# Kernel optimization log

Hardware: AMD Instinct MI355X
Metric: run time of the kernel (lower is better)

Reference implementation:

```python
import jax, jax.numpy as jnp
from jax import lax
import numpy as np

N = 4
ALPHA_AP = 0.85
ALPHA_DS = 0.1
ALPHA_LR = 1.0
C1 = 0.01 ** 2
C2 = 0.03 ** 2


def resize_ac(img, nh, nw):
    # bilinear resize, align_corners=True (matches F.interpolate(..., align_corners=True))
    B, C, H, W = img.shape
    ys = jnp.linspace(0.0, H - 1.0, nh)
    xs = jnp.linspace(0.0, W - 1.0, nw)
    y0 = jnp.floor(ys).astype(jnp.int32)
    y1 = jnp.minimum(y0 + 1, H - 1)
    x0 = jnp.floor(xs).astype(jnp.int32)
    x1 = jnp.minimum(x0 + 1, W - 1)
    wy = (ys - y0).astype(img.dtype)[None, None, :, None]
    wx = (xs - x0).astype(img.dtype)[None, None, None, :]
    top = img[:, :, y0, :] * (1.0 - wy) + img[:, :, y1, :] * wy
    return top[:, :, :, x0] * (1.0 - wx) + top[:, :, :, x1] * wx


def build_pyramid(img):
    B, C, H, W = img.shape
    pyr = [img]
    for i in range(N - 1):
        r = 2 ** (i + 1)
        pyr.append(resize_ac(pyr[i], H // r, W // r))  # resize previous level, as in torch code
    return pyr


def x_grad(img):
    # replicate-pad right then diff -> last column is exactly zero
    g = img[:, :, :, :-1] - img[:, :, :, 1:]
    return jnp.concatenate([g, jnp.zeros_like(img[:, :, :, :1])], axis=3)


def y_grad(img):
    g = img[:, :, :-1, :] - img[:, :, 1:, :]
    return jnp.concatenate([g, jnp.zeros_like(img[:, :, :1, :])], axis=2)


def avgpool3(x):
    # AvgPool2d(3, 1), VALID padding
    return lax.reduce_window(x, 0.0, lax.add, (1, 1, 3, 3), (1, 1, 1, 1), 'VALID') / 9.0


def grid_sample_zeros(img, gx, gy):
    # bilinear grid_sample, padding_mode='zeros', align_corners=True
    B, C, H, W = img.shape
    x = (gx + 1.0) * 0.5 * (W - 1)
    y = (gy + 1.0) * 0.5 * (H - 1)
    x0 = jnp.floor(x)
    y0 = jnp.floor(y)

    def corner(xi, yi, w):
        valid = (xi >= 0) & (xi <= W - 1) & (yi >= 0) & (yi <= H - 1)
        xc = jnp.clip(xi, 0, W - 1).astype(jnp.int32)
        yc = jnp.clip(yi, 0, H - 1).astype(jnp.int32)
        vals = jax.vmap(lambda im, yy, xx: im[:, yy, xx])(img, yc, xc)  # [B,C,H,W]
        return vals * (w * valid.astype(img.dtype))[:, None]

    return (corner(x0, y0, (x0 + 1 - x) * (y0 + 1 - y))
            + corner(x0 + 1, y0, (x - x0) * (y0 + 1 - y))
            + corner(x0, y0 + 1, (x0 + 1 - x) * (y - y0))
            + corner(x0 + 1, y0 + 1, (x - x0) * (y - y0)))


def apply_disparity(img, disp):
    # standard Monodepth bilinear sampler: shift x_base in [0,1] by disp, grid_sample
    B, C, H, W = img.shape
    x_base = jnp.linspace(0.0, 1.0, W)[None, None, :]
    y_base = jnp.linspace(0.0, 1.0, H)[None, :, None]
    gx = 2.0 * (x_base + disp[:, 0]) - 1.0  # [B,H,W]
    gy = jnp.broadcast_to(2.0 * y_base - 1.0, gx.shape)
    return grid_sample_zeros(img, gx, gy)


def dssim(x, y):
    mu_x = avgpool3(x)
    mu_y = avgpool3(y)
    sig_x = avgpool3(x * x) - mu_x ** 2
    sig_y = avgpool3(y * y) - mu_y ** 2
    cov = avgpool3(x * y) - mu_x * mu_y
    ssim = ((2.0 * mu_x * mu_y + C1) * (2.0 * cov + C2)) / ((mu_x ** 2 + mu_y ** 2 + C1) * (sig_x + sig_y + C2))
    return jnp.mean(jnp.clip((1.0 - ssim) / 2.0, 0.0, 1.0))


def smoothness(disp, img, level):
    wx = jnp.exp(-jnp.mean(jnp.abs(x_grad(img)), axis=1, keepdims=True))
    wy = jnp.exp(-jnp.mean(jnp.abs(y_grad(img)), axis=1, keepdims=True))
    sx = x_grad(disp) * wx
    sy = y_grad(disp) * wy
    return jnp.mean(jnp.abs(sx) + jnp.abs(sy)) / (2 ** level)


def loss_forward(disps, left, right):
    lp = build_pyramid(left)
    rp = build_pyramid(right)
    dl = [d[:, 0:1] for d in disps]
    dr = [d[:, 1:2] for d in disps]
    left_est = [apply_disparity(rp[i], -dl[i]) for i in range(N)]
    right_est = [apply_disparity(lp[i], dr[i]) for i in range(N)]
    r2l_disp = [apply_disparity(dr[i], -dl[i]) for i in range(N)]
    l2r_disp = [apply_disparity(dl[i], dr[i]) for i in range(N)]
    # appearance matching (note: outer *ALPHA_AP matches the original's AP_loss*self.alpha_AP)
    AP = sum(ALPHA_AP * dssim(lp[i], left_est[i]) + (1.0 - ALPHA_AP) * jnp.mean(jnp.abs(lp[i] - left_est[i])) for i in range(N))
    AP = AP + sum(ALPHA_AP * dssim(rp[i], right_est[i]) + (1.0 - ALPHA_AP) * jnp.mean(jnp.abs(rp[i] - right_est[i])) for i in range(N))
    AP = AP * ALPHA_AP
    LR = sum(jnp.mean(jnp.abs(dl[i] - r2l_disp[i])) for i in range(N))
    LR = (LR + sum(jnp.mean(jnp.abs(dr[i] - l2r_disp[i])) for i in range(N))) * ALPHA_LR
    DS = sum(smoothness(dl[i], lp[i], i) for i in range(N))
    DS = (DS + sum(smoothness(dr[i], rp[i], i) for i in range(N))) * ALPHA_DS
    total = AP + LR + DS
    return total, AP, LR, DS


def setup_inputs() -> dict:
    key = jax.random.key(0)
    ks = jax.random.split(key, 6)
    B, H, W = 32, 256, 512
    inp = {}
    for i in range(N):
        h, w = H >> i, W >> i
        # normalized disparities in [0, 0.05) as in trained Monodepth
        inp[f'disp{i}'] = jax.random.uniform(ks[i], (B, 2, h, w), jnp.float32) * 0.05
    inp['left'] = jax.random.uniform(ks[4], (B, 3, H, W), jnp.float32)
    inp['right'] = jax.random.uniform(ks[5], (B, 3, H, W), jnp.float32)
    return inp


def reference(disp0, disp1, disp2, disp3, left, right):
    return loss_forward([disp0, disp1, disp2, disp3], left, right)
```

## Files before the change

### kernel.cpp

```cpp
#include <hip/hip_runtime.h>

#define BDIM 256
#define SH 16

struct LevelDesc {
    const float* lp; const float* rp; const float* dp;
    int H, W, nCW, nRS, nPerSide, waveBase;
};
struct AllParams { LevelDesc lv[4]; int totalWaves; };

__global__ void zero_acc_kernel(double* acc) {
    if (threadIdx.x < 32) acc[threadIdx.x] = 0.0;
}

__global__ void resize2_kernel(const float* __restrict__ sL, const float* __restrict__ sR,
                               float* __restrict__ dL, float* __restrict__ dR,
                               int BC, int Hs, int Ws, int Hd, int Wd) {
    long long half = (long long)BC * Hd * Wd;
    long long idx = (long long)blockIdx.x * blockDim.x + threadIdx.x;
    if (idx >= 2 * half) return;
    const float* src = (idx < half) ? sL : sR;
    float* dst = (idx < half) ? dL : dR;
    long long id = (idx < half) ? idx : idx - half;
    int i = (int)(id % Wd);
    long long t = id / Wd;
    int j = (int)(t % Hd);
    int bc = (int)(t / Hd);
    float stepy = (float)(Hs - 1) / (float)(Hd - 1);
    float stepx = (float)(Ws - 1) / (float)(Wd - 1);
    float y = j * stepy;
    float x = i * stepx;
    int y0 = (int)floorf(y);
    int y1 = min(y0 + 1, Hs - 1);
    int x0 = (int)floorf(x);
    int x1 = min(x0 + 1, Ws - 1);
    float wy = y - (float)y0;
    float wx = x - (float)x0;
    const float* s = src + (long long)bc * Hs * Ws;
    float t0 = s[(long long)y0 * Ws + x0] * (1.0f - wy) + s[(long long)y1 * Ws + x0] * wy;
    float t1 = s[(long long)y0 * Ws + x1] * (1.0f - wy) + s[(long long)y1 * Ws + x1] * wy;
    dst[id] = t0 * (1.0f - wx) + t1 * wx;
}

__device__ __forceinline__ float ssim_term(float Sx, float Sy, float Sxx, float Syy, float Sxy) {
    const float C1v = 0.0001f;
    const float C2v = 0.0009f;
    float mux = Sx * (1.0f / 9.0f), muy = Sy * (1.0f / 9.0f);
    float sigx = Sxx * (1.0f / 9.0f) - mux * mux;
    float sigy = Syy * (1.0f / 9.0f) - muy * muy;
    float cov  = Sxy * (1.0f / 9.0f) - mux * muy;
    float num = (2.0f * mux * muy + C1v) * (2.0f * cov + C2v);
    float den = (mux * mux + muy * muy + C1v) * (sigx + sigy + C2v);
    float v = (1.0f - num * __builtin_amdgcn_rcpf(den)) * 0.5f;
    return fminf(fmaxf(v, 0.0f), 1.0f);
}

__global__ void __launch_bounds__(BDIM)
mega_kernel(AllParams P, double* __restrict__ acc) {
    const int lane = threadIdx.x & 63;
    const int wid  = threadIdx.x >> 6;
    const int wId  = blockIdx.x * (BDIM / 64) + wid;
    const int w = min(wId, P.totalWaves - 1);

    int level = 0;
    if (w >= P.lv[1].waveBase) level = 1;
    if (w >= P.lv[2].waveBase) level = 2;
    if (w >= P.lv[3].waveBase) level = 3;
    LevelDesc L;
    if (level == 0) L = P.lv[0];
    else if (level == 1) L = P.lv[1];
    else if (level == 2) L = P.lv[2];
    else L = P.lv[3];

    int rel = w - L.waveBase;
    const int side = (rel >= L.nPerSide) ? 1 : 0;
    rel -= side * L.nPerSide;
    const int cw = rel % L.nCW; rel /= L.nCW;
    const int rs = rel % L.nRS;
    const int b  = rel / L.nRS;

    const int H = L.H, W = L.W;
    const long long HW = (long long)H * W;
    const float Wm1f = (float)(W - 1);
    const float sgn = side ? 1.0f : -1.0f;

    const float* xim = (side ? L.rp : L.lp) + (long long)b * 3 * HW;
    const float* sim = (side ? L.lp : L.rp) + (long long)b * 3 * HW;
    const float* dme = L.dp + (long long)b * 2 * HW + (side ? HW : 0);
    const float* dot = L.dp + (long long)b * 2 * HW + (side ? 0 : HW);

    const int base = cw * 126;
    const int c0 = base + 2 * lane;
    const int c1 = c0 + 1;
    const bool in0 = c0 < W, in1 = c1 < W;
    const int cc = min(c0, W - 2) >> 1;
    const float fc0 = (float)c0, fc1 = (float)c1;

    const bool lastW = (cw == L.nCW - 1);
    const bool own0 = in0 && (c0 < base + 126 || lastW);
    const bool own1 = in1 && (c1 < base + 126 || lastW);
    const bool ownS0 = own0 && (c0 <= W - 3);
    const bool ownS1 = own1 && (c1 <= W - 3);

    const int r0 = rs * SH;
    const int r1 = min(r0 + SH, H);
    const int jend = min(r1 + 1, H - 1);

    float Pst[3][5][2], Lst[3][5][2];
#pragma unroll
    for (int c = 0; c < 3; ++c)
#pragma unroll
        for (int s = 0; s < 5; ++s) { Pst[c][s][0] = 0.f; Pst[c][s][1] = 0.f;
                                      Lst[c][s][0] = 0.f; Lst[c][s][1] = 0.f; }
    float pd0 = 0.f, pd1 = 0.f;
    float pxv[3][2] = {{0.f,0.f},{0.f,0.f},{0.f,0.f}};

    float f_ss = 0.f, f_l1 = 0.f, f_lr = 0.f, f_ds = 0.f;

    for (int j = r0; j <= jend; ++j) {
        const long long ro = (long long)j * W;
        float2 dpair = ((const float2*)(dme + ro))[cc];
        float d0 = dpair.x, d1 = dpair.y;

        float xq0 = fmaf(sgn * d0, Wm1f, fc0);
        float xq1 = fmaf(sgn * d1, Wm1f, fc1);
        float xf0 = floorf(xq0), xf1 = floorf(xq1);
        int g0 = (int)xf0, g1 = (int)xf1;
        float t0 = xq0 - xf0, t1 = xq1 - xf1;
        float w00 = (g0 >= 0 && g0 < W)         ? 1.0f - t0 : 0.0f;
        float w01 = (g0 >= -1 && g0 < W - 1)    ? t0        : 0.0f;
        float w10 = (g1 >= 0 && g1 < W)         ? 1.0f - t1 : 0.0f;
        float w11 = (g1 >= -1 && g1 < W - 1)    ? t1        : 0.0f;
        int a0 = min(max(g0, 0), W - 1);
        int a1 = min(max(g0 + 1, 0), W - 1);
        int b0 = min(max(g1, 0), W - 1);
        int b1 = min(max(g1 + 1, 0), W - 1);

        const float* dor = dot + ro;
        float wv0 = dor[a0] * w00 + dor[a1] * w01;
        float wv1 = dor[b0] * w10 + dor[b1] * w11;

        float xv[3][2], yv[3][2];
#pragma unroll
        for (int c = 0; c < 3; ++c) {
            const float* xr = xim + (long long)c * HW + ro;
            const float* sr = sim + (long long)c * HW + ro;
            float2 xp2 = ((const float2*)xr)[cc];
            xv[c][0] = in0 ? xp2.x : 0.f;
            xv[c][1] = in1 ? xp2.y : 0.f;
            yv[c][0] = sr[a0] * w00 + sr[a1] * w01;
            yv[c][1] = sr[b0] * w10 + sr[b1] * w11;
            if (!in0) yv[c][0] = 0.f;
            if (!in1) yv[c][1] = 0.f;
        }

        const bool rowOwn = j < r1;
        if (rowOwn) {
            if (own0) {
                f_l1 += fabsf(xv[0][0] - yv[0][0]) + fabsf(xv[1][0] - yv[1][0]) + fabsf(xv[2][0] - yv[2][0]);
                f_lr += fabsf(d0 - wv0);
            }
            if (own1) {
                f_l1 += fabsf(xv[0][1] - yv[0][1]) + fabsf(xv[1][1] - yv[1][1]) + fabsf(xv[2][1] - yv[2][1]);
                f_lr += fabsf(d1 - wv1);
            }
        }

        {
            float dn  = __shfl_down(d0, 1);
            float xn0 = __shfl_down(xv[0][0], 1);
            float xn1 = __shfl_down(xv[1][0], 1);
            float xn2 = __shfl_down(xv[2][0], 1);
            if (rowOwn) {
                if (own0 && c0 < W - 1) {
                    float g = fabsf(xv[0][0] - xv[0][1]) + fabsf(xv[1][0] - xv[1][1]) + fabsf(xv[2][0] - xv[2][1]);
                    f_ds += fabsf((d0 - d1) * __expf(-g * (1.0f / 3.0f)));
                }
                if (own1 && c1 < W - 1) {
                    float g = fabsf(xv[0][1] - xn0) + fabsf(xv[1][1] - xn1) + fabsf(xv[2][1] - xn2);
                    f_ds += fabsf((d1 - dn) * __expf(-g * (1.0f / 3.0f)));
                }
            }
        }
        if (j > r0 && (j - 1) < r1) {
            if (own0) {
                float g = fabsf(pxv[0][0] - xv[0][0]) + fabsf(pxv[1][0] - xv[1][0]) + fabsf(pxv[2][0] - xv[2][0]);
                f_ds += fabsf((pd0 - d0) * __expf(-g * (1.0f / 3.0f)));
            }
            if (own1) {
                float g = fabsf(pxv[0][1] - xv[0][1]) + fabsf(pxv[1][1] - xv[1][1]) + fabsf(pxv[2][1] - xv[2][1]);
                f_ds += fabsf((pd1 - d1) * __expf(-g * (1.0f / 3.0f)));
            }
        }
        pd0 = d0; pd1 = d1;
#pragma unroll
        for (int c = 0; c < 3; ++c) { pxv[c][0] = xv[c][0]; pxv[c][1] = xv[c][1]; }

        const bool emit = (j >= r0 + 2);
#pragma unroll
        for (int c = 0; c < 3; ++c) {
            float cs[5][2];
#pragma unroll
            for (int p = 0; p < 2; ++p) {
                float cx = xv[c][p], cy = yv[c][p];
                float v5[5] = {cx, cy, cx * cx, cy * cy, cx * cy};
#pragma unroll
                for (int s = 0; s < 5; ++s) {
                    cs[s][p] = Pst[c][s][p] + v5[s];
                    Pst[c][s][p] = Lst[c][s][p] + v5[s];
                    Lst[c][s][p] = v5[s];
                }
            }
            if (emit) {
                float w0s[5], w1s[5];
#pragma unroll
                for (int s = 0; s < 5; ++s) {
                    float n0 = __shfl_down(cs[s][0], 1);
                    float n1 = __shfl_down(cs[s][1], 1);
                    w0s[s] = cs[s][0] + cs[s][1] + n0;
                    w1s[s] = cs[s][1] + n0 + n1;
                }
                float ts0 = ssim_term(w0s[0], w0s[1], w0s[2], w0s[3], w0s[4]);
                float ts1 = ssim_term(w1s[0], w1s[1], w1s[2], w1s[3], w1s[4]);
                f_ss += (ownS0 ? ts0 : 0.f) + (ownS1 ? ts1 : 0.f);
            }
        }
    }

#pragma unroll
    for (int o = 32; o > 0; o >>= 1) {
        f_ss += __shfl_down(f_ss, o);
        f_l1 += __shfl_down(f_l1, o);
        f_lr += __shfl_down(f_lr, o);
        f_ds += __shfl_down(f_ds, o);
    }
    __shared__ float red[BDIM / 64][4];
    __shared__ int meta[2];
    if (threadIdx.x == 0) { meta[0] = level; meta[1] = side; }
    if (lane == 0) {
        red[wid][0] = f_ss; red[wid][1] = f_l1;
        red[wid][2] = f_lr; red[wid][3] = f_ds;
    }
    __syncthreads();
    if (threadIdx.x < 4) {
        int t = threadIdx.x;
        double s = (double)red[0][t] + (double)red[1][t]
                 + (double)red[2][t] + (double)red[3][t];
        atomicAdd(acc + t * 8 + meta[1] * 4 + meta[0], s);
    }
}

__global__ void finalize_kernel(const double* __restrict__ acc, float* __restrict__ out) {
    const int B = 32, H0 = 256, W0 = 512;
    double AP = 0.0, LR = 0.0, DS = 0.0;
    for (int i = 0; i < 4; ++i) {
        int h = H0 >> i, w = W0 >> i;
        double nss = (double)B * 3.0 * (double)(h - 2) * (double)(w - 2);
        double nl1 = (double)B * 3.0 * (double)h * (double)w;
        double nd  = (double)B * (double)h * (double)w;
        AP += 0.85 * (acc[0 + i] / nss) + 0.15 * (acc[8 + i] / nl1);
        AP += 0.85 * (acc[4 + i] / nss) + 0.15 * (acc[12 + i] / nl1);
        LR += acc[16 + i] / nd + acc[20 + i] / nd;
        double sc = 1.0 / (double)(1 << i);
        DS += (acc[24 + i] / nd) * sc + (acc[28 + i] / nd) * sc;
    }
    AP *= 0.85;
    DS *= 0.1;
    double total = AP + LR + DS;
    out[0] = (float)total;
    out[1] = (float)AP;
    out[2] = (float)LR;
    out[3] = (float)DS;
}

extern "C" void kernel_launch(void* const* d_in, const int* in_sizes, int n_in,
                              void* d_out, int out_size, void* d_ws, size_t ws_size,
                              hipStream_t stream) {
    const int B = 32, H0 = 256, W0 = 512;
    const float* dsp[4];
    for (int i = 0; i < 4; ++i) dsp[i] = (const float*)d_in[i];
    const float* left  = (const float*)d_in[4];
    const float* right = (const float*)d_in[5];
    float* out = (float*)d_out;

    double* acc = (double*)d_ws;
    float* buf = (float*)((char*)d_ws + 256);

    const float* lp[4];
    const float* rp[4];
    float* lpm[4];
    float* rpm[4];
    lp[0] = left; rp[0] = right;
    float* cur = buf;
    for (int i = 1; i < 4; ++i) { lpm[i] = cur; cur += (long long)B * 3 * (H0 >> i) * (W0 >> i); }
    for (int i = 1; i < 4; ++i) { rpm[i] = cur; cur += (long long)B * 3 * (H0 >> i) * (W0 >> i); }
    for (int i = 1; i < 4; ++i) { lp[i] = lpm[i]; rp[i] = rpm[i]; }

    zero_acc_kernel<<<1, 64, 0, stream>>>(acc);

    for (int i = 1; i < 4; ++i) {
        int Hs = H0 >> (i - 1), Ws = W0 >> (i - 1);
        int Hd = H0 >> i, Wd = W0 >> i;
        long long half = (long long)B * 3 * Hd * Wd;
        int g = (int)((2 * half + BDIM - 1) / BDIM);
        resize2_kernel<<<g, BDIM, 0, stream>>>(
            lp[i - 1], rp[i - 1], lpm[i], rpm[i], B * 3, Hs, Ws, Hd, Wd);
    }

    AllParams P;
    int wb = 0;
    for (int i = 0; i < 4; ++i) {
        int h = H0 >> i, w = W0 >> i;
        LevelDesc& L = P.lv[i];
        L.lp = lp[i]; L.rp = rp[i]; L.dp = dsp[i];
        L.H = h; L.W = w;
        L.nCW = (w - 2 + 125) / 126;
        L.nRS = h / SH;
        L.nPerSide = B * L.nRS * L.nCW;
        L.waveBase = wb;
        wb += 2 * L.nPerSide;
    }
    P.totalWaves = wb;
    int blocks = (wb + (BDIM / 64) - 1) / (BDIM / 64);
    mega_kernel<<<blocks, BDIM, 0, stream>>>(P, acc);

    finalize_kernel<<<1, 1, 0, stream>>>(acc, out);
}
```

Measured before the change: 302.0 us.

## Software-pipeline row gathers with double-buffered registers and 32-bit indexing

Restructures the per-row loop so the disparity load and all gathers for row j+1 (and the disparity for row j+2) are issued before row j is consumed. Two register sets alternate between rows so memory latency can overlap with the SSIM and smoothness math. Address arithmetic also switches from 64-bit to 32-bit unsigned offsets. The cost is much higher register pressure, which may lower occupancy, and 32-bit offsets assume each tensor slice fits in 4G elements.

Result: slower. 308.6 us (+2.2%).

```diff
diff --git a/kernel.cpp b/kernel.cpp
--- a/kernel.cpp
+++ b/kernel.cpp
@@ -55,6 +55,14 @@
     return fminf(fmaxf(v, 0.0f), 1.0f);
 }
 
+struct RowVals {
+    float d0, d1;
+    float xv[3][2];
+    float w00, w01, w10, w11;
+    float dA, dB, dC, dD;
+    float sA[3], sB[3], sC[3], sD[3];
+};
+
 __global__ void __launch_bounds__(BDIM)
 mega_kernel(AllParams P, double* __restrict__ acc) {
     const int lane = threadIdx.x & 63;
@@ -81,6 +89,7 @@
 
     const int H = L.H, W = L.W;
     const long long HW = (long long)H * W;
+    const unsigned HWu = (unsigned)HW;
     const float Wm1f = (float)(W - 1);
     const float sgn = side ? 1.0f : -1.0f;
 
@@ -117,41 +126,51 @@
 
     float f_ss = 0.f, f_l1 = 0.f, f_lr = 0.f, f_ds = 0.f;
 
-    for (int j = r0; j <= jend; ++j) {
-        const long long ro = (long long)j * W;
-        float2 dpair = ((const float2*)(dme + ro))[cc];
-        float d0 = dpair.x, d1 = dpair.y;
-
-        float xq0 = fmaf(sgn * d0, Wm1f, fc0);
-        float xq1 = fmaf(sgn * d1, Wm1f, fc1);
+    auto load_dp = [&](int jj, float& o0, float& o1) {
+        float2 dpair = ((const float2*)(dme + (unsigned)jj * (unsigned)W))[cc];
+        o0 = dpair.x; o1 = dpair.y;
+    };
+
+    auto issue_gathers = [&](float di0, float di1, int jj, RowVals& R) {
+        const unsigned ro = (unsigned)jj * (unsigned)W;
+        R.d0 = di0; R.d1 = di1;
+        float xq0 = fmaf(sgn * di0, Wm1f, fc0);
+        float xq1 = fmaf(sgn * di1, Wm1f, fc1);
         float xf0 = floorf(xq0), xf1 = floorf(xq1);
         int g0 = (int)xf0, g1 = (int)xf1;
         float t0 = xq0 - xf0, t1 = xq1 - xf1;
-        float w00 = (g0 >= 0 && g0 < W)         ? 1.0f - t0 : 0.0f;
-        float w01 = (g0 >= -1 && g0 < W - 1)    ? t0        : 0.0f;
-        float w10 = (g1 >= 0 && g1 < W)         ? 1.0f - t1 : 0.0f;
-        float w11 = (g1 >= -1 && g1 < W - 1)    ? t1        : 0.0f;
-        int a0 = min(max(g0, 0), W - 1);
-        int a1 = min(max(g0 + 1, 0), W - 1);
-        int b0 = min(max(g1, 0), W - 1);
-        int b1 = min(max(g1 + 1, 0), W - 1);
-
-        const float* dor = dot + ro;
-        float wv0 = dor[a0] * w00 + dor[a1] * w01;
-        float wv1 = dor[b0] * w10 + dor[b1] * w11;
-
+        R.w00 = (g0 >= 0 && g0 < W)         ? 1.0f - t0 : 0.0f;
+        R.w01 = (g0 >= -1 && g0 < W - 1)    ? t0        : 0.0f;
+        R.w10 = (g1 >= 0 && g1 < W)         ? 1.0f - t1 : 0.0f;
+        R.w11 = (g1 >= -1 && g1 < W - 1)    ? t1        : 0.0f;
+        unsigned a0 = ro + (unsigned)min(max(g0, 0), W - 1);
+        unsigned a1 = ro + (unsigned)min(max(g0 + 1, 0), W - 1);
+        unsigned b0 = ro + (unsigned)min(max(g1, 0), W - 1);
+        unsigned b1 = ro + (unsigned)min(max(g1 + 1, 0), W - 1);
+        R.dA = dot[a0]; R.dB = dot[a1]; R.dC = dot[b0]; R.dD = dot[b1];
+#pragma unroll
+        for (int c = 0; c < 3; ++c) {
+            const unsigned co = (unsigned)c * HWu;
+            float2 xp2 = ((const float2*)(xim + co + ro))[cc];
+            R.xv[c][0] = in0 ? xp2.x : 0.f;
+            R.xv[c][1] = in1 ? xp2.y : 0.f;
+            R.sA[c] = sim[co + a0]; R.sB[c] = sim[co + a1];
+            R.sC[c] = sim[co + b0]; R.sD[c] = sim[co + b1];
+        }
+    };
+
+    auto consume = [&](const RowVals& R, int j) {
+        const float d0 = R.d0, d1 = R.d1;
+        float wv0 = R.dA * R.w00 + R.dB * R.w01;
+        float wv1 = R.dC * R.w10 + R.dD * R.w11;
         float xv[3][2], yv[3][2];
 #pragma unroll
         for (int c = 0; c < 3; ++c) {
-            const float* xr = xim + (long long)c * HW + ro;
-            const float* sr = sim + (long long)c * HW + ro;
-            float2 xp2 = ((const float2*)xr)[cc];
-            xv[c][0] = in0 ? xp2.x : 0.f;
-            xv[c][1] = in1 ? xp2.y : 0.f;
-            yv[c][0] = sr[a0] * w00 + sr[a1] * w01;
-            yv[c][1] = sr[b0] * w10 + sr[b1] * w11;
-            if (!in0) yv[c][0] = 0.f;
-            if (!in1) yv[c][1] = 0.f;
+            xv[c][0] = R.xv[c][0]; xv[c][1] = R.xv[c][1];
+            float ya = R.sA[c] * R.w00 + R.sB[c] * R.w01;
+            float yb = R.sC[c] * R.w10 + R.sD[c] * R.w11;
+            yv[c][0] = in0 ? ya : 0.f;
+            yv[c][1] = in1 ? yb : 0.f;
         }
 
         const bool rowOwn = j < r1;
@@ -225,6 +244,28 @@
                 f_ss += (ownS0 ? ts0 : 0.f) + (ownS1 ? ts1 : 0.f);
             }
         }
+    };
+
+    RowVals A, B;
+    float dq0, dq1, dn0, dn1;
+    load_dp(r0, dq0, dq1);
+    load_dp(min(r0 + 1, jend), dn0, dn1);
+    issue_gathers(dq0, dq1, r0, A);
+
+    int j = r0;
+    for (;;) {
+        float dp20, dp21;
+        load_dp(min(j + 2, jend), dp20, dp21);
+        if (j < jend) issue_gathers(dn0, dn1, j + 1, B);
+        consume(A, j);
+        dn0 = dp20; dn1 = dp21;
+        if (++j > jend) break;
+
+        load_dp(min(j + 2, jend), dp20, dp21);
+        if (j < jend) issue_gathers(dn0, dn1, j + 1, A);
+        consume(B, j);
+        dn0 = dp20; dn1 = dp21;
+        if (++j > jend) break;
     }
 
 #pragma unroll
```
